# Performance work log

Measured on AMD Instinct MI355X. Metric: run time of the kernel, lower is better.

The kernel has to match this reference:

```python
import jax, jax.numpy as jnp
import numpy as np

N = 50000        # nodes
E = 800000       # edges
G = 256          # graphs in batch
DIMS = [128, 128, 64, 32]
BN_EPS = 1e-5
TEMP = 5.0


def setup_inputs() -> dict:
    key = jax.random.key(0)
    ks = iter(jax.random.split(key, 32))
    inp = {}
    inp["x"] = jax.random.normal(next(ks), (N, DIMS[0]), dtype=jnp.float32)
    inp["edge_index"] = jax.random.randint(next(ks), (2, E), 0, N)
    inp["batch"] = jnp.sort(jax.random.randint(next(ks), (N,), 0, G))
    for i in range(3):
        din, dout = DIMS[i], DIMS[i + 1]
        inp[f"W1_{i}"] = jax.random.normal(next(ks), (din, dout), dtype=jnp.float32) * 0.05
        inp[f"b1_{i}"] = jnp.zeros((dout,), jnp.float32)
        inp[f"W2_{i}"] = jax.random.normal(next(ks), (dout, dout), dtype=jnp.float32) * 0.05
        inp[f"b2_{i}"] = jnp.zeros((dout,), jnp.float32)
        inp[f"gamma_{i}"] = jnp.ones((dout,), jnp.float32)
        inp[f"beta_{i}"] = jnp.zeros((dout,), jnp.float32)
        inp[f"mean_{i}"] = jnp.zeros((dout,), jnp.float32)
        inp[f"var_{i}"] = jnp.ones((dout,), jnp.float32)
    inp["W_lin"] = jax.random.normal(next(ks), (DIMS[3], 1), dtype=jnp.float32) * 0.05
    inp["b_lin"] = jnp.zeros((1,), jnp.float32)
    return inp


def _gin_bn(x, src, dst, W1, b1, W2, b2, g, b, m, v):
    # GINConv with eps=0: h_i = MLP(x_i + sum_{j->i} x_j), then BatchNorm (eval)
    agg = jax.ops.segment_sum(x[src], dst, num_segments=N)  # [N, din]
    h = x + agg
    h = jnp.maximum(h @ W1 + b1, 0.0) @ W2 + b2             # 2-layer MLP
    return (h - m) * jax.lax.rsqrt(v + BN_EPS) * g + b


def reference(x, edge_index, batch,
              W1_0, b1_0, W2_0, b2_0, gamma_0, beta_0, mean_0, var_0,
              W1_1, b1_1, W2_1, b2_1, gamma_1, beta_1, mean_1, var_1,
              W1_2, b1_2, W2_2, b2_2, gamma_2, beta_2, mean_2, var_2,
              W_lin, b_lin):
    src, dst = edge_index[0], edge_index[1]
    layers = [
        (W1_0, b1_0, W2_0, b2_0, gamma_0, beta_0, mean_0, var_0),
        (W1_1, b1_1, W2_1, b2_1, gamma_1, beta_1, mean_1, var_1),
        (W1_2, b1_2, W2_2, b2_2, gamma_2, beta_2, mean_2, var_2),
    ]
    for i, p in enumerate(layers):
        x = _gin_bn(x, src, dst, *p)
        if i != len(layers) - 1:
            x = jnp.maximum(x, 0.0)  # relu; dropout is identity in eval mode
    logits = (x @ W_lin + b_lin) / TEMP                      # [N, 1]
    # per-graph (segment) softmax over nodes
    mx = jax.ops.segment_max(logits, batch, num_segments=G)  # [G, 1]
    e = jnp.exp(logits - mx[batch])
    s = jax.ops.segment_sum(e, batch, num_segments=G)        # [G, 1]
    return e / s[batch]
```

## Files before the change

kernel.cpp:

```cpp
#include <hip/hip_runtime.h>

#define NN 50000
#define NE 800000
#define NG 256
#define N4 (NN * 128 / 4)
#define NQ (NE / 4)
#define CB 64
#define QPB (NQ / CB)
#define NBK 196

typedef __attribute__((ext_vector_type(8))) short bf16x8;
typedef __attribute__((ext_vector_type(4))) float f32x4;

__device__ __forceinline__ unsigned short f2bf_rne(float f) {
    unsigned u = __float_as_uint(f);
    u += 0x7fffu + ((u >> 16) & 1u);
    return (unsigned short)(u >> 16);
}
#define BF2F_LO(u) __uint_as_float((u) << 16)
#define BF2F_HI(u) __uint_as_float((u) & 0xffff0000u)

__global__ void conv_count(const float4* __restrict__ x, ushort4* __restrict__ xh,
                           const int4* __restrict__ dst4, int* __restrict__ cnt1) {
    __shared__ int hist[NBK];
    int i = blockIdx.x * 256 + threadIdx.x;
    if (i < N4) {
        float4 v = x[i];
        ushort4 o;
        o.x = f2bf_rne(v.x); o.y = f2bf_rne(v.y);
        o.z = f2bf_rne(v.z); o.w = f2bf_rne(v.w);
        xh[i] = o;
    }
    if (blockIdx.x < CB) {
        int t = threadIdx.x;
        if (t < NBK) hist[t] = 0;
        __syncthreads();
        int qb = blockIdx.x * QPB;
        for (int qi = t; qi < QPB; qi += 256) {
            int4 d = dst4[qb + qi];
            atomicAdd(&hist[d.x >> 8], 1);
            atomicAdd(&hist[d.y >> 8], 1);
            atomicAdd(&hist[d.z >> 8], 1);
            atomicAdd(&hist[d.w >> 8], 1);
        }
        __syncthreads();
        if (t < NBK) cnt1[blockIdx.x * NBK + t] = hist[t];
    }
}

__global__ __launch_bounds__(256) void scan_buckets(
        const int* __restrict__ cnt1, int* __restrict__ off1,
        int* __restrict__ bstart, int* __restrict__ rowptr) {
    __shared__ int c[CB * NBK];
    __shared__ int sh[256];
    int t = threadIdx.x;
    for (int idx = t; idx < CB * NBK; idx += 256) c[idx] = cnt1[idx];
    __syncthreads();
    int tot = 0;
    if (t < NBK) {
        for (int b = 0; b < CB; b++) {
            int v = c[b * NBK + t];
            c[b * NBK + t] = tot;
            tot += v;
        }
    }
    sh[t] = (t < NBK) ? tot : 0;
    __syncthreads();
    int v = sh[t];
    #pragma unroll
    for (int off = 1; off < 256; off <<= 1) {
        int add = (t >= off) ? sh[t - off] : 0;
        __syncthreads();
        sh[t] += add;
        __syncthreads();
    }
    int excl = sh[t] - v;
    if (t < NBK) {
        bstart[t] = excl;
        for (int b = 0; b < CB; b++) c[b * NBK + t] += excl;
    }
    if (t == 0) { bstart[NBK] = NE; rowptr[NN] = NE; }
    __syncthreads();
    for (int idx = t; idx < CB * NBK; idx += 256) off1[idx] = c[idx];
}

__global__ __launch_bounds__(256) void scatter1(
        const int4* __restrict__ src4, const int4* __restrict__ dst4,
        const int* __restrict__ off1, int2* __restrict__ tmp) {
    __shared__ int curs[NBK];
    int t = threadIdx.x;
    if (t < NBK) curs[t] = off1[blockIdx.x * NBK + t];
    __syncthreads();
    int qb = blockIdx.x * QPB;
    for (int qi = t; qi < QPB; qi += 256) {
        int4 s = src4[qb + qi];
        int4 d = dst4[qb + qi];
        int p0 = atomicAdd(&curs[d.x >> 8], 1);
        int p1 = atomicAdd(&curs[d.y >> 8], 1);
        int p2 = atomicAdd(&curs[d.z >> 8], 1);
        int p3 = atomicAdd(&curs[d.w >> 8], 1);
        tmp[p0] = make_int2(s.x, d.x);
        tmp[p1] = make_int2(s.y, d.y);
        tmp[p2] = make_int2(s.z, d.z);
        tmp[p3] = make_int2(s.w, d.w);
    }
}

__global__ __launch_bounds__(256) void bucket_build(
        const int2* __restrict__ tmp, const int* __restrict__ bstart,
        const int* __restrict__ batch, int* __restrict__ rowptr,
        int* __restrict__ gstart, int* __restrict__ esrc,
        const float* __restrict__ W1, const float* __restrict__ W2,
        const float* __restrict__ W3,
        const float* __restrict__ W21, const float* __restrict__ W12,
        unsigned short* __restrict__ W1t, unsigned short* __restrict__ W2t,
        unsigned short* __restrict__ W3t, unsigned short* __restrict__ W21t,
        unsigned short* __restrict__ W12t) {
    int gidx = blockIdx.x * 256 + threadIdx.x;
    if (gidx < 16384) {
        int n = gidx >> 7, k = gidx & 127;
        W1t[gidx] = f2bf_rne(W1[k * 128 + n]);
        W2t[gidx] = f2bf_rne(W2[k * 128 + n]);
    } else if (gidx < 24576) {
        int i2 = gidx - 16384;
        int n = i2 >> 7, k = i2 & 127;
        W3t[i2] = f2bf_rne(W3[k * 64 + n]);
    } else if (gidx < 28672) {
        int i3 = gidx - 24576;
        int n = i3 >> 6, k = i3 & 63;
        W21t[i3] = f2bf_rne(W21[k * 64 + n]);
    } else if (gidx < 30720) {
        int i4 = gidx - 28672;
        int n = i4 >> 6, k = i4 & 63;
        W12t[i4] = f2bf_rne(W12[k * 32 + n]);
    }

    __shared__ int hist[256];
    __shared__ int sh[256];
    __shared__ int curs[256];
    int t = threadIdx.x, k1 = blockIdx.x;
    int b0 = bstart[k1], b1v = bstart[k1 + 1];
    int cnt = b1v - b0;
    hist[t] = 0;
    __syncthreads();
    for (int e = t; e < cnt; e += 256) {
        int2 sd = tmp[b0 + e];
        atomicAdd(&hist[sd.y & 255], 1);
    }
    __syncthreads();
    int v = hist[t];
    sh[t] = v;
    __syncthreads();
    #pragma unroll
    for (int off = 1; off < 256; off <<= 1) {
        int add = (t >= off) ? sh[t - off] : 0;
        __syncthreads();
        sh[t] += add;
        __syncthreads();
    }
    int excl = sh[t] - v;
    int node = k1 * 256 + t;
    if (node < NN) {
        rowptr[node] = b0 + excl;
        int b = batch[node];
        if (node == 0) {
            for (int g = 0; g <= b; g++) gstart[g] = 0;
        } else {
            int p = batch[node - 1];
            for (int g = p + 1; g <= b; g++) gstart[g] = node;
        }
        if (node == NN - 1) {
            for (int g = b + 1; g <= NG; g++) gstart[g] = NN;
        }
    }
    curs[t] = b0 + excl;
    __syncthreads();
    for (int e = t; e < cnt; e += 256) {
        int2 sd = tmp[b0 + e];
        int slot = atomicAdd(&curs[sd.y & 255], 1);
        esrc[slot] = sd.x;
    }
}


template <int C4>
__device__ __forceinline__ void gather_bf16(const uint4* __restrict__ x4,
                                            const int* __restrict__ esrc,
                                            int beg, int cnt, int node, int lane,
                                            float* a ) {
    constexpr int EPI = 64 / C4;
    const int chunk = lane & (C4 - 1);
    const int esl   = lane / C4;
    #define ACC_U4(u) do { \
        a[0] += BF2F_LO((u).x); a[1] += BF2F_HI((u).x); \
        a[2] += BF2F_LO((u).y); a[3] += BF2F_HI((u).y); \
        a[4] += BF2F_LO((u).z); a[5] += BF2F_HI((u).z); \
        a[6] += BF2F_LO((u).w); a[7] += BF2F_HI((u).w); } while (0)
    if (esl == 0) { uint4 u = x4[(size_t)node * C4 + chunk]; ACC_U4(u); }
    for (int c = 0; c < cnt; c += 64) {
        int take = min(64, cnt - c);
        int myi = (lane < take) ? esrc[beg + c + lane] : 0;
        int i = 0;
        for (; i + 4 * EPI <= take; i += 4 * EPI) {
            int s0 = __shfl(myi, i + esl);
            int s1 = __shfl(myi, i + EPI + esl);
            int s2 = __shfl(myi, i + 2 * EPI + esl);
            int s3 = __shfl(myi, i + 3 * EPI + esl);
            uint4 u0 = x4[(size_t)s0 * C4 + chunk];
            uint4 u1 = x4[(size_t)s1 * C4 + chunk];
            uint4 u2 = x4[(size_t)s2 * C4 + chunk];
            uint4 u3 = x4[(size_t)s3 * C4 + chunk];
            ACC_U4(u0); ACC_U4(u1); ACC_U4(u2); ACC_U4(u3);
        }
        if (i + 2 * EPI <= take) {
            int s0 = __shfl(myi, i + esl);
            int s1 = __shfl(myi, i + EPI + esl);
            uint4 u0 = x4[(size_t)s0 * C4 + chunk];
            uint4 u1 = x4[(size_t)s1 * C4 + chunk];
            ACC_U4(u0); ACC_U4(u1);
            i += 2 * EPI;
        }
        if (i + EPI <= take) {
            int s = __shfl(myi, i + esl);
            uint4 u = x4[(size_t)s * C4 + chunk];
            ACC_U4(u);
            i += EPI;
        }
        int rem = take - i;
        if (rem > 0) {
            int s = __shfl(myi, i + ((esl < rem) ? esl : 0));
            uint4 u = x4[(size_t)s * C4 + chunk];
            if (esl < rem) ACC_U4(u);
        }
    }
    #undef ACC_U4
    for (int off = 32; off >= C4; off >>= 1) {
        #pragma unroll
        for (int q = 0; q < 8; q++)
            a[q] += __shfl_xor(a[q], off);
    }
}

template <int C>
__device__ __forceinline__ void gather_bf16_u2(const uint2* __restrict__ x2,
                                               const int* __restrict__ esrc,
                                               int beg, int cnt, int node, int lane,
                                               float* a ) {
    constexpr int EPI = 64 / C;
    const int chunk = lane & (C - 1);
    const int esl   = lane / C;
    #define ACC_U2(u) do { \
        a[0] += BF2F_LO((u).x); a[1] += BF2F_HI((u).x); \
        a[2] += BF2F_LO((u).y); a[3] += BF2F_HI((u).y); } while (0)
    if (esl == 0) { uint2 u = x2[(size_t)node * C + chunk]; ACC_U2(u); }
    for (int c = 0; c < cnt; c += 64) {
        int take = min(64, cnt - c);
        int myi = (lane < take) ? esrc[beg + c + lane] : 0;
        int i = 0;
        for (; i + 4 * EPI <= take; i += 4 * EPI) {
            int s0 = __shfl(myi, i + esl);
            int s1 = __shfl(myi, i + EPI + esl);
            int s2 = __shfl(myi, i + 2 * EPI + esl);
            int s3 = __shfl(myi, i + 3 * EPI + esl);
            uint2 u0 = x2[(size_t)s0 * C + chunk];
            uint2 u1 = x2[(size_t)s1 * C + chunk];
            uint2 u2 = x2[(size_t)s2 * C + chunk];
            uint2 u3 = x2[(size_t)s3 * C + chunk];
            ACC_U2(u0); ACC_U2(u1); ACC_U2(u2); ACC_U2(u3);
        }
        if (i + 2 * EPI <= take) {
            int s0 = __shfl(myi, i + esl);
            int s1 = __shfl(myi, i + EPI + esl);
            uint2 u0 = x2[(size_t)s0 * C + chunk];
            uint2 u1 = x2[(size_t)s1 * C + chunk];
            ACC_U2(u0); ACC_U2(u1);
            i += 2 * EPI;
        }
        if (i + EPI <= take) {
            int s = __shfl(myi, i + esl);
            uint2 u = x2[(size_t)s * C + chunk];
            ACC_U2(u);
            i += EPI;
        }
        int rem = take - i;
        if (rem > 0) {
            int s = __shfl(myi, i + ((esl < rem) ? esl : 0));
            uint2 u = x2[(size_t)s * C + chunk];
            if (esl < rem) ACC_U2(u);
        }
    }
    #undef ACC_U2
    for (int off = 32; off >= C; off >>= 1) {
        #pragma unroll
        for (int q = 0; q < 4; q++)
            a[q] += __shfl_xor(a[q], off);
    }
}

template <int C>
__device__ __forceinline__ void gather_bf16_u1(const unsigned* __restrict__ x1,
                                               const int* __restrict__ esrc,
                                               int beg, int cnt, int node, int lane,
                                               float* a ) {
    constexpr int EPI = 64 / C;
    const int chunk = lane & (C - 1);
    const int esl   = lane / C;
    #define ACC_U1(u) do { \
        a[0] += BF2F_LO(u); a[1] += BF2F_HI(u); } while (0)
    if (esl == 0) { unsigned u = x1[(size_t)node * C + chunk]; ACC_U1(u); }
    for (int c = 0; c < cnt; c += 64) {
        int take = min(64, cnt - c);
        int myi = (lane < take) ? esrc[beg + c + lane] : 0;
        int i = 0;
        for (; i + 4 * EPI <= take; i += 4 * EPI) {
            int s0 = __shfl(myi, i + esl);
            int s1 = __shfl(myi, i + EPI + esl);
            int s2 = __shfl(myi, i + 2 * EPI + esl);
            int s3 = __shfl(myi, i + 3 * EPI + esl);
            unsigned u0 = x1[(size_t)s0 * C + chunk];
            unsigned u1 = x1[(size_t)s1 * C + chunk];
            unsigned u2 = x1[(size_t)s2 * C + chunk];
            unsigned u3 = x1[(size_t)s3 * C + chunk];
            ACC_U1(u0); ACC_U1(u1); ACC_U1(u2); ACC_U1(u3);
        }
        if (i + 2 * EPI <= take) {
            int s0 = __shfl(myi, i + esl);
            int s1 = __shfl(myi, i + EPI + esl);
            unsigned u0 = x1[(size_t)s0 * C + chunk];
            unsigned u1 = x1[(size_t)s1 * C + chunk];
            ACC_U1(u0); ACC_U1(u1);
            i += 2 * EPI;
        }
        if (i + EPI <= take) {
            int s = __shfl(myi, i + esl);
            unsigned u = x1[(size_t)s * C + chunk];
            ACC_U1(u);
            i += EPI;
        }
        int rem = take - i;
        if (rem > 0) {
            int s = __shfl(myi, i + ((esl < rem) ? esl : 0));
            unsigned u = x1[(size_t)s * C + chunk];
            if (esl < rem) ACC_U1(u);
        }
    }
    #undef ACC_U1
    for (int off = 32; off >= C; off >>= 1) {
        #pragma unroll
        for (int q = 0; q < 2; q++)
            a[q] += __shfl_xor(a[q], off);
    }
}

__global__ __launch_bounds__(256) void gather_L0(
        const unsigned short* __restrict__ xh, const int* __restrict__ esrc,
        const int* __restrict__ rowptr, unsigned short* __restrict__ aggh ) {
    const int wave = threadIdx.x >> 6, lane = threadIdx.x & 63;
    const int node = blockIdx.x * 4 + wave;
    if (node >= NN) return;
    float a[8] = {0, 0, 0, 0, 0, 0, 0, 0};
    int beg = rowptr[node], end = rowptr[node + 1];
    gather_bf16<16>((const uint4*)xh, esrc, beg, end - beg, node, lane, a);
    if (lane < 16) {
        uint4 o;
        o.x = (unsigned)f2bf_rne(a[0]) | ((unsigned)f2bf_rne(a[1]) << 16);
        o.y = (unsigned)f2bf_rne(a[2]) | ((unsigned)f2bf_rne(a[3]) << 16);
        o.z = (unsigned)f2bf_rne(a[4]) | ((unsigned)f2bf_rne(a[5]) << 16);
        o.w = (unsigned)f2bf_rne(a[6]) | ((unsigned)f2bf_rne(a[7]) << 16);
        *(uint4*)&aggh[(size_t)node * 128 + lane * 8] = o;
    }
}

__global__ __launch_bounds__(256) void gather_L1(
        const unsigned short* __restrict__ z1h, const int* __restrict__ esrc,
        const int* __restrict__ rowptr, const float* __restrict__ b1,
        unsigned short* __restrict__ agg1h ) {
    const int wave = threadIdx.x >> 6, lane = threadIdx.x & 63;
    const int node = blockIdx.x * 4 + wave;
    if (node >= NN) return;
    float a[4] = {0, 0, 0, 0};
    int beg = rowptr[node], end = rowptr[node + 1];
    gather_bf16_u2<16>((const uint2*)z1h, esrc, beg, end - beg, node, lane, a);
    if (lane < 16) {
        float4 bv = *(const float4*)&b1[lane * 4];
        uint2 o;
        o.x = (unsigned)f2bf_rne(fmaxf(a[0] + bv.x, 0.f)) |
              ((unsigned)f2bf_rne(fmaxf(a[1] + bv.y, 0.f)) << 16);
        o.y = (unsigned)f2bf_rne(fmaxf(a[2] + bv.z, 0.f)) |
              ((unsigned)f2bf_rne(fmaxf(a[3] + bv.w, 0.f)) << 16);
        *(uint2*)&agg1h[(size_t)node * 64 + lane * 4] = o;
    }
}

__global__ __launch_bounds__(256) void gather_L2(
        const unsigned short* __restrict__ z2h, const int* __restrict__ esrc,
        const int* __restrict__ rowptr, const float* __restrict__ b1,
        unsigned short* __restrict__ agg2h ) {
    const int wave = threadIdx.x >> 6, lane = threadIdx.x & 63;
    const int node = blockIdx.x * 4 + wave;
    if (node >= NN) return;
    float a[2] = {0, 0};
    int beg = rowptr[node], end = rowptr[node + 1];
    gather_bf16_u1<16>((const unsigned*)z2h, esrc, beg, end - beg, node, lane, a);
    if (lane < 16) {
        float2 bv = *(const float2*)&b1[lane * 2];
        unsigned o = (unsigned)f2bf_rne(fmaxf(a[0] + bv.x, 0.f)) |
                     ((unsigned)f2bf_rne(fmaxf(a[1] + bv.y, 0.f)) << 16);
        *(unsigned*)&agg2h[(size_t)node * 32 + lane * 2] = o;
    }
}

__global__ __launch_bounds__(256) void gemm_L0(
        const unsigned short* __restrict__ aggh, unsigned short* __restrict__ z1h,
        const unsigned short* __restrict__ W1t,
        const unsigned short* __restrict__ W2t,
        const unsigned short* __restrict__ W3t,
        const float* __restrict__ b1, const float* __restrict__ b2,
        const float* __restrict__ gamma, const float* __restrict__ beta,
        const float* __restrict__ mean, const float* __restrict__ var) {
    constexpr int MT = 64, LDA = 136;
    __shared__ __align__(16) unsigned short shA[MT * LDA];
    __shared__ __align__(16) unsigned short shB[MT * LDA];
    const int tid = threadIdx.x;
    const int wave = tid >> 6, lane = tid & 63;
    const int nodeBase = blockIdx.x * MT;
    const int lr = lane & 15;
    const int lg = lane >> 4;
    const int lk = lg * 8;
    const int n0 = wave * 32;

    #pragma unroll
    for (int j = 0; j < 4; j++) {
        int f = tid + j * 256;
        int row = f >> 4, c = f & 15;
        int node = nodeBase + row;
        uint4 v = (node < NN) ? ((const uint4*)aggh)[(size_t)node * 16 + c]
                              : make_uint4(0u, 0u, 0u, 0u);
        *(uint4*)&shA[row * LDA + c * 8] = v;
    }
    __syncthreads();

    f32x4 acc[4][2];

    {
        float bv0 = b1[n0 + lr], bv1 = b1[n0 + 16 + lr];
        #pragma unroll
        for (int m = 0; m < 4; m++) {
            f32x4 c0 = {bv0, bv0, bv0, bv0};
            f32x4 c1 = {bv1, bv1, bv1, bv1};
            acc[m][0] = c0; acc[m][1] = c1;
        }
        #pragma unroll
        for (int ks = 0; ks < 4; ks++) {
            const int k0 = ks * 32 + lk;
            bf16x8 wb0 = *(const bf16x8*)&W1t[(n0 + lr) * 128 + k0];
            bf16x8 wb1 = *(const bf16x8*)&W1t[(n0 + 16 + lr) * 128 + k0];
            #pragma unroll
            for (int m = 0; m < 4; m++) {
                bf16x8 af = *(const bf16x8*)&shA[(m * 16 + lr) * LDA + k0];
                acc[m][0] = __builtin_amdgcn_mfma_f32_16x16x32_bf16(af, wb0, acc[m][0], 0, 0, 0);
                acc[m][1] = __builtin_amdgcn_mfma_f32_16x16x32_bf16(af, wb1, acc[m][1], 0, 0, 0);
            }
        }
    }
    #pragma unroll
    for (int m = 0; m < 4; m++) {
        #pragma unroll
        for (int nt = 0; nt < 2; nt++) {
            #pragma unroll
            for (int r = 0; r < 4; r++) {
                shB[(m * 16 + lg * 4 + r) * LDA + (n0 + nt * 16 + lr)] =
                    f2bf_rne(fmaxf(acc[m][nt][r], 0.f));
            }
        }
    }
    __syncthreads();

    {
        float bv0 = b2[n0 + lr], bv1 = b2[n0 + 16 + lr];
        #pragma unroll
        for (int m = 0; m < 4; m++) {
            f32x4 c0 = {bv0, bv0, bv0, bv0};
            f32x4 c1 = {bv1, bv1, bv1, bv1};
            acc[m][0] = c0; acc[m][1] = c1;
        }
        #pragma unroll
        for (int ks = 0; ks < 4; ks++) {
            const int k0 = ks * 32 + lk;
            bf16x8 wb0 = *(const bf16x8*)&W2t[(n0 + lr) * 128 + k0];
            bf16x8 wb1 = *(const bf16x8*)&W2t[(n0 + 16 + lr) * 128 + k0];
            #pragma unroll
            for (int m = 0; m < 4; m++) {
                bf16x8 af = *(const bf16x8*)&shB[(m * 16 + lr) * LDA + k0];
                acc[m][0] = __builtin_amdgcn_mfma_f32_16x16x32_bf16(af, wb0, acc[m][0], 0, 0, 0);
                acc[m][1] = __builtin_amdgcn_mfma_f32_16x16x32_bf16(af, wb1, acc[m][1], 0, 0, 0);
            }
        }
    }
    float s0 = gamma[n0 + lr]      * (1.0f / sqrtf(var[n0 + lr] + 1e-5f));
    float t0 = beta[n0 + lr]       - mean[n0 + lr] * s0;
    float s1 = gamma[n0 + 16 + lr] * (1.0f / sqrtf(var[n0 + 16 + lr] + 1e-5f));
    float t1 = beta[n0 + 16 + lr]  - mean[n0 + 16 + lr] * s1;
    #pragma unroll
    for (int m = 0; m < 4; m++) {
        #pragma unroll
        for (int nt = 0; nt < 2; nt++) {
            float sc = nt ? s1 : s0, sf = nt ? t1 : t0;
            #pragma unroll
            for (int r = 0; r < 4; r++) {
                float y = fmaxf(fmaf(acc[m][nt][r], sc, sf), 0.f);
                shA[(m * 16 + lg * 4 + r) * LDA + (n0 + nt * 16 + lr)] = f2bf_rne(y);
            }
        }
    }
    __syncthreads();

    f32x4 a3[4];
    #pragma unroll
    for (int m = 0; m < 4; m++) {
        f32x4 z = {0.f, 0.f, 0.f, 0.f};
        a3[m] = z;
    }
    #pragma unroll
    for (int ks = 0; ks < 4; ks++) {
        const int k0 = ks * 32 + lk;
        bf16x8 wb = *(const bf16x8*)&W3t[(wave * 16 + lr) * 128 + k0];
        #pragma unroll
        for (int m = 0; m < 4; m++) {
            bf16x8 af = *(const bf16x8*)&shA[(m * 16 + lr) * LDA + k0];
            a3[m] = __builtin_amdgcn_mfma_f32_16x16x32_bf16(af, wb, a3[m], 0, 0, 0);
        }
    }
    #pragma unroll
    for (int m = 0; m < 4; m++) {
        #pragma unroll
        for (int r = 0; r < 4; r++) {
            int node = nodeBase + m * 16 + lg * 4 + r;
            if (node < NN)
                z1h[(size_t)node * 64 + wave * 16 + lr] = f2bf_rne(a3[m][r]);
        }
    }
}

__global__ __launch_bounds__(256) void gemm_L1(
        const unsigned short* __restrict__ agg1h, unsigned short* __restrict__ z2h,
        const unsigned short* __restrict__ W21t,
        const unsigned short* __restrict__ W12t,
        const float* __restrict__ b2, const float* __restrict__ gamma,
        const float* __restrict__ beta, const float* __restrict__ mean,
        const float* __restrict__ var) {
    constexpr int MT = 64, LDA = 72;
    __shared__ __align__(16) unsigned short shA[MT * LDA];
    __shared__ __align__(16) unsigned short shB[MT * LDA];
    const int tid = threadIdx.x;
    const int wave = tid >> 6, lane = tid & 63;
    const int nodeBase = blockIdx.x * MT;
    const int lr = lane & 15;
    const int lg = lane >> 4;
    const int lk = lg * 8;
    const int n0 = wave * 16;

    #pragma unroll
    for (int j = 0; j < 2; j++) {
        int f = tid + j * 256;
        int row = f >> 3, c = f & 7;
        int node = nodeBase + row;
        uint4 v = (node < NN) ? ((const uint4*)agg1h)[(size_t)node * 8 + c]
                              : make_uint4(0u, 0u, 0u, 0u);
        *(uint4*)&shA[row * LDA + c * 8] = v;
    }
    __syncthreads();

    f32x4 acc[4];
    {
        float bv = b2[n0 + lr];
        #pragma unroll
        for (int m = 0; m < 4; m++) {
            f32x4 c0 = {bv, bv, bv, bv};
            acc[m] = c0;
        }
        #pragma unroll
        for (int ks = 0; ks < 2; ks++) {
            const int k0 = ks * 32 + lk;
            bf16x8 wb = *(const bf16x8*)&W21t[(n0 + lr) * 64 + k0];
            #pragma unroll
            for (int m = 0; m < 4; m++) {
                bf16x8 af = *(const bf16x8*)&shA[(m * 16 + lr) * LDA + k0];
                acc[m] = __builtin_amdgcn_mfma_f32_16x16x32_bf16(af, wb, acc[m], 0, 0, 0);
            }
        }
    }
    float sc = gamma[n0 + lr] * (1.0f / sqrtf(var[n0 + lr] + 1e-5f));
    float sf = beta[n0 + lr] - mean[n0 + lr] * sc;
    #pragma unroll
    for (int m = 0; m < 4; m++) {
        #pragma unroll
        for (int r = 0; r < 4; r++) {
            float y = fmaxf(fmaf(acc[m][r], sc, sf), 0.f);
            shB[(m * 16 + lg * 4 + r) * LDA + (n0 + lr)] = f2bf_rne(y);
        }
    }
    __syncthreads();

    const int rh = (wave >> 1) * 32, ch = (wave & 1) * 16;
    f32x4 a3[2];
    {
        f32x4 z = {0.f, 0.f, 0.f, 0.f};
        a3[0] = z; a3[1] = z;
    }
    #pragma unroll
    for (int ks = 0; ks < 2; ks++) {
        const int k0 = ks * 32 + lk;
        bf16x8 wb = *(const bf16x8*)&W12t[(ch + lr) * 64 + k0];
        #pragma unroll
        for (int m = 0; m < 2; m++) {
            bf16x8 af = *(const bf16x8*)&shB[(rh + m * 16 + lr) * LDA + k0];
            a3[m] = __builtin_amdgcn_mfma_f32_16x16x32_bf16(af, wb, a3[m], 0, 0, 0);
        }
    }
    #pragma unroll
    for (int m = 0; m < 2; m++) {
        #pragma unroll
        for (int r = 0; r < 4; r++) {
            int node = nodeBase + rh + m * 16 + lg * 4 + r;
            if (node < NN)
                z2h[(size_t)node * 32 + ch + lr] = f2bf_rne(a3[m][r]);
        }
    }
}

__global__ __launch_bounds__(256) void gemm_L2(
        const unsigned short* __restrict__ agg2h, float* __restrict__ logits,
        const float* __restrict__ W2, const float* __restrict__ b2,
        const float* __restrict__ gamma, const float* __restrict__ beta,
        const float* __restrict__ mean, const float* __restrict__ var,
        const float* __restrict__ Wl, const float* __restrict__ bl) {
    constexpr int MT = 32, LD = 36;
    __shared__ float sh[MT * LD];
    const int tid = threadIdx.x;
    const int nodeBase = blockIdx.x * MT;

    {
        int row = tid >> 3, c = tid & 7;
        int node = nodeBase + row;
        uint2 v = (node < NN) ? ((const uint2*)agg2h)[(size_t)node * 8 + c]
                              : make_uint2(0u, 0u);
        sh[row * LD + c * 4 + 0] = BF2F_LO(v.x);
        sh[row * LD + c * 4 + 1] = BF2F_HI(v.x);
        sh[row * LD + c * 4 + 2] = BF2F_LO(v.y);
        sh[row * LD + c * 4 + 3] = BF2F_HI(v.y);
    }
    __syncthreads();

    const int colid = tid % 8, rowid = tid / 8;
    const int c0 = colid * 4, r0 = rowid;
    float acc[4];
    {
        float4 bv = *(const float4*)&b2[c0];
        acc[0] = bv.x; acc[1] = bv.y; acc[2] = bv.z; acc[3] = bv.w;
        #pragma unroll
        for (int k4 = 0; k4 < 8; k4++) {
            float4 w[4];
            #pragma unroll
            for (int kk = 0; kk < 4; kk++)
                w[kk] = *(const float4*)&W2[(k4 * 4 + kk) * 32 + c0];
            float4 a = *(const float4*)&sh[r0 * LD + k4 * 4];
            const float av[4] = {a.x, a.y, a.z, a.w};
            #pragma unroll
            for (int kk = 0; kk < 4; kk++) {
                const float* wp = (const float*)&w[kk];
                #pragma unroll
                for (int j = 0; j < 4; j++)
                    acc[j] = fmaf(av[kk], wp[j], acc[j]);
            }
        }
    }
    float4 gv = *(const float4*)&gamma[c0];
    float4 bev = *(const float4*)&beta[c0];
    float4 mv = *(const float4*)&mean[c0];
    float4 vv = *(const float4*)&var[c0];
    float4 wl = *(const float4*)&Wl[c0];
    float p = 0.f;
    {
        const float* gp = (const float*)&gv; const float* bp = (const float*)&bev;
        const float* mp = (const float*)&mv; const float* vp = (const float*)&vv;
        const float* wp = (const float*)&wl;
        #pragma unroll
        for (int j = 0; j < 4; j++) {
            float sc = gp[j] * (1.0f / sqrtf(vp[j] + 1e-5f));
            float y = (acc[j] - mp[j]) * sc + bp[j];
            p = fmaf(y, wp[j], p);
        }
    }
    p += __shfl_xor(p, 1);
    p += __shfl_xor(p, 2);
    p += __shfl_xor(p, 4);
    int node = nodeBase + r0;
    if ((tid & 7) == 0 && node < NN)
        logits[node] = (p + bl[0]) * 0.2f;
}

__global__ __launch_bounds__(256) void seg_softmax(
        const float* __restrict__ logits, const int* __restrict__ gstart,
        float* __restrict__ out) {
    __shared__ float slog[1024];
    __shared__ float sred[4];
    __shared__ float sbc[2];
    int g = blockIdx.x;
    int beg = gstart[g], end = gstart[g + 1];
    int cnt = end - beg;
    int t = threadIdx.x;
    if (cnt <= 0) return;
    bool fits = (cnt <= 1024);

    float lmax = -3.402823466e+38f;
    for (int i = t; i < cnt; i += 256) {
        float lg = logits[beg + i];
        if (fits) slog[i] = lg;
        lmax = fmaxf(lmax, lg);
    }
    #pragma unroll
    for (int off = 32; off > 0; off >>= 1)
        lmax = fmaxf(lmax, __shfl_down(lmax, off));
    if ((t & 63) == 0) sred[t >> 6] = lmax;
    __syncthreads();
    if (t == 0) sbc[0] = fmaxf(fmaxf(sred[0], sred[1]), fmaxf(sred[2], sred[3]));
    __syncthreads();
    float gm = sbc[0];

    float lsum = 0.f;
    for (int i = t; i < cnt; i += 256) {
        float lg = fits ? slog[i] : logits[beg + i];
        float e = expf(lg - gm);
        if (fits) slog[i] = e;
        lsum += e;
    }
    #pragma unroll
    for (int off = 32; off > 0; off >>= 1)
        lsum += __shfl_down(lsum, off);
    __syncthreads();
    if ((t & 63) == 0) sred[t >> 6] = lsum;
    __syncthreads();
    if (t == 0) sbc[1] = (sred[0] + sred[1]) + (sred[2] + sred[3]);
    __syncthreads();
    float inv = 1.0f / sbc[1];

    for (int i = t; i < cnt; i += 256) {
        float e = fits ? slog[i] : expf(logits[beg + i] - gm);
        out[beg + i] = e * inv;
    }
}

extern "C" void kernel_launch(void* const* d_in, const int* in_sizes, int n_in,
                              void* d_out, int out_size, void* d_ws, size_t ws_size,
                              hipStream_t stream) {
    const float* x    = (const float*)d_in[0];
    const int*   ei   = (const int*)d_in[1];
    const int*   srcI = ei;
    const int*   dstI = ei + NE;
    const int*   batch = (const int*)d_in[2];

    const float* P[29];
    for (int i = 0; i < 29; i++) P[i] = (const float*)d_in[i];
    const float* Wlin = P[27];
    const float* blin = P[28];

    unsigned short* xh  = (unsigned short*)d_ws;
    unsigned short* z1h = xh + (size_t)NN * 128;
    unsigned short* z2h = z1h + (size_t)NN * 64;
    float* logits = (float*)(z2h + (size_t)NN * 32);
    int* gstart = (int*)(logits + NN);
    int* rowptr = gstart + NG + 1;
    int* cnt1   = rowptr + NN + 1;
    int* off1   = cnt1 + CB * NBK;
    int* bstart = off1 + CB * NBK;
    uintptr_t tal = ((uintptr_t)(bstart + NBK + 1) + 15) & ~(uintptr_t)15;
    int2* tmp   = (int2*)tal;
    int* esrc   = (int*)(tmp + NE);
    uintptr_t pal = ((uintptr_t)(esrc + NE) + 255) & ~(uintptr_t)255;
    unsigned short* aggh  = (unsigned short*)pal;
    unsigned short* W1t   = aggh + (size_t)NN * 128;
    unsigned short* W2t   = W1t + 16384;
    unsigned short* W3t   = W2t + 16384;
    unsigned short* W21t  = W3t + 8192;
    unsigned short* W12t  = W21t + 4096;
    unsigned short* agg1h = W12t + 2048;
    unsigned short* agg2h = agg1h + (size_t)NN * 64;
    float* outp = (float*)d_out;

    const int TB = 256;

    conv_count<<<(N4 + TB - 1) / TB, TB, 0, stream>>>(
        (const float4*)x, (ushort4*)xh, (const int4*)dstI, cnt1);
    scan_buckets<<<1, 256, 0, stream>>>(cnt1, off1, bstart, rowptr);
    scatter1<<<CB, 256, 0, stream>>>(
        (const int4*)srcI, (const int4*)dstI, off1, tmp);
    bucket_build<<<NBK, 256, 0, stream>>>(tmp, bstart, batch, rowptr, gstart, esrc,
        P[3], P[5], P[11], P[13], P[19], W1t, W2t, W3t, W21t, W12t);

    const int GB   = (NN + 3) / 4;
    const int FB64 = (NN + 63) / 64;
    const int FB32 = (NN + 31) / 32;

    gather_L0<<<GB, 256, 0, stream>>>(xh, esrc, rowptr, aggh);
    gemm_L0<<<FB64, 256, 0, stream>>>(aggh, z1h, W1t, W2t, W3t,
        P[4], P[6], P[7], P[8], P[9], P[10]);
    gather_L1<<<GB, 256, 0, stream>>>(z1h, esrc, rowptr, P[12], agg1h);
    gemm_L1<<<FB64, 256, 0, stream>>>(agg1h, z2h, W21t, W12t,
        P[14], P[15], P[16], P[17], P[18]);
    gather_L2<<<GB, 256, 0, stream>>>(z2h, esrc, rowptr, P[20], agg2h);
    gemm_L2<<<FB32, 256, 0, stream>>>(agg2h, logits,
        P[21], P[22], P[23], P[24], P[25], P[26], Wlin, blin);

    seg_softmax<<<NG, 256, 0, stream>>>(logits, gstart, outp);
}
```

Before: 262.3 us.

## Fold bucket scan into scatter and build kernels; pack edge temp into 32 bits

Removes the single-block scan_buckets kernel. Each scatter1 and bucket_build block now reloads the full count table and recomputes the bucket prefix sums it needs. The intermediate edge buffer changes from int2 (src, dst) to a single 32-bit word holding the 16-bit source and the low 8 bits of the destination, halving its write and read traffic. The cost is a redundant scan in every block, a 50KB shared-memory table per block, and reliance on node ids fitting in 16 bits.

```diff
diff --git a/kernel.cpp b/kernel.cpp
--- a/kernel.cpp
+++ b/kernel.cpp
@@ -48,23 +48,25 @@
     }
 }
 
-__global__ __launch_bounds__(256) void scan_buckets(
-        const int* __restrict__ cnt1, int* __restrict__ off1,
-        int* __restrict__ bstart, int* __restrict__ rowptr) {
+__global__ __launch_bounds__(256) void scatter1(
+        const int4* __restrict__ src4, const int4* __restrict__ dst4,
+        const int* __restrict__ cnt1, unsigned* __restrict__ tmp) {
     __shared__ int c[CB * NBK];
     __shared__ int sh[256];
+    __shared__ int curs[256];
     int t = threadIdx.x;
     for (int idx = t; idx < CB * NBK; idx += 256) c[idx] = cnt1[idx];
     __syncthreads();
-    int tot = 0;
+    int myoff = 0, tv = 0;
     if (t < NBK) {
+        int run = 0;
         for (int b = 0; b < CB; b++) {
-            int v = c[b * NBK + t];
-            c[b * NBK + t] = tot;
-            tot += v;
-        }
-    }
-    sh[t] = (t < NBK) ? tot : 0;
+            if (b == (int)blockIdx.x) myoff = run;
+            run += c[b * NBK + t];
+        }
+        tv = run;
+    }
+    sh[t] = tv;
     __syncthreads();
     int v = sh[t];
     #pragma unroll
@@ -75,21 +77,7 @@
         __syncthreads();
     }
     int excl = sh[t] - v;
-    if (t < NBK) {
-        bstart[t] = excl;
-        for (int b = 0; b < CB; b++) c[b * NBK + t] += excl;
-    }
-    if (t == 0) { bstart[NBK] = NE; rowptr[NN] = NE; }
-    __syncthreads();
-    for (int idx = t; idx < CB * NBK; idx += 256) off1[idx] = c[idx];
-}
-
-__global__ __launch_bounds__(256) void scatter1(
-        const int4* __restrict__ src4, const int4* __restrict__ dst4,
-        const int* __restrict__ off1, int2* __restrict__ tmp) {
-    __shared__ int curs[NBK];
-    int t = threadIdx.x;
-    if (t < NBK) curs[t] = off1[blockIdx.x * NBK + t];
+    if (t < NBK) curs[t] = excl + myoff;
     __syncthreads();
     int qb = blockIdx.x * QPB;
     for (int qi = t; qi < QPB; qi += 256) {
@@ -99,15 +87,15 @@
         int p1 = atomicAdd(&curs[d.y >> 8], 1);
         int p2 = atomicAdd(&curs[d.z >> 8], 1);
         int p3 = atomicAdd(&curs[d.w >> 8], 1);
-        tmp[p0] = make_int2(s.x, d.x);
-        tmp[p1] = make_int2(s.y, d.y);
-        tmp[p2] = make_int2(s.z, d.z);
-        tmp[p3] = make_int2(s.w, d.w);
+        tmp[p0] = (unsigned)s.x | ((unsigned)(d.x & 255) << 16);
+        tmp[p1] = (unsigned)s.y | ((unsigned)(d.y & 255) << 16);
+        tmp[p2] = (unsigned)s.z | ((unsigned)(d.z & 255) << 16);
+        tmp[p3] = (unsigned)s.w | ((unsigned)(d.w & 255) << 16);
     }
 }
 
 __global__ __launch_bounds__(256) void bucket_build(
-        const int2* __restrict__ tmp, const int* __restrict__ bstart,
+        const unsigned* __restrict__ tmp, const int* __restrict__ cnt1,
         const int* __restrict__ batch, int* __restrict__ rowptr,
         int* __restrict__ gstart, int* __restrict__ esrc,
         const float* __restrict__ W1, const float* __restrict__ W2,
@@ -135,17 +123,43 @@
         W12t[i4] = f2bf_rne(W12[k * 32 + n]);
     }
 
+    __shared__ int c[CB * NBK];
+    __shared__ int tot[256];
+    __shared__ int pre[256];
     __shared__ int hist[256];
     __shared__ int sh[256];
     __shared__ int curs[256];
     int t = threadIdx.x, k1 = blockIdx.x;
-    int b0 = bstart[k1], b1v = bstart[k1 + 1];
-    int cnt = b1v - b0;
+
+    for (int idx = t; idx < CB * NBK; idx += 256) c[idx] = cnt1[idx];
+    __syncthreads();
+    int tv = 0;
+    if (t < NBK) {
+        int run = 0;
+        for (int b = 0; b < CB; b++) run += c[b * NBK + t];
+        tv = run;
+    }
+    tot[t] = tv;
+    sh[t] = tv;
+    __syncthreads();
+    int v0 = sh[t];
+    #pragma unroll
+    for (int off = 1; off < 256; off <<= 1) {
+        int add = (t >= off) ? sh[t - off] : 0;
+        __syncthreads();
+        sh[t] += add;
+        __syncthreads();
+    }
+    pre[t] = sh[t] - v0;
+    __syncthreads();
+    const int b0 = pre[k1];
+    const int cnt = tot[k1];
+
     hist[t] = 0;
     __syncthreads();
     for (int e = t; e < cnt; e += 256) {
-        int2 sd = tmp[b0 + e];
-        atomicAdd(&hist[sd.y & 255], 1);
+        unsigned pk = tmp[b0 + e];
+        atomicAdd(&hist[pk >> 16], 1);
     }
     __syncthreads();
     int v = hist[t];
@@ -173,12 +187,13 @@
             for (int g = b + 1; g <= NG; g++) gstart[g] = NN;
         }
     }
+    if (k1 == 0 && t == 0) rowptr[NN] = NE;
     curs[t] = b0 + excl;
     __syncthreads();
     for (int e = t; e < cnt; e += 256) {
-        int2 sd = tmp[b0 + e];
-        int slot = atomicAdd(&curs[sd.y & 255], 1);
-        esrc[slot] = sd.x;
+        unsigned pk = tmp[b0 + e];
+        int slot = atomicAdd(&curs[pk >> 16], 1);
+        esrc[slot] = (int)(pk & 0xffffu);
     }
 }
 
@@ -772,10 +787,8 @@
     int* gstart = (int*)(logits + NN);
     int* rowptr = gstart + NG + 1;
     int* cnt1   = rowptr + NN + 1;
-    int* off1   = cnt1 + CB * NBK;
-    int* bstart = off1 + CB * NBK;
-    uintptr_t tal = ((uintptr_t)(bstart + NBK + 1) + 15) & ~(uintptr_t)15;
-    int2* tmp   = (int2*)tal;
+    uintptr_t tal = ((uintptr_t)(cnt1 + CB * NBK) + 15) & ~(uintptr_t)15;
+    unsigned* tmp = (unsigned*)tal;
     int* esrc   = (int*)(tmp + NE);
     uintptr_t pal = ((uintptr_t)(esrc + NE) + 255) & ~(uintptr_t)255;
     unsigned short* aggh  = (unsigned short*)pal;
@@ -792,10 +805,9 @@
 
     conv_count<<<(N4 + TB - 1) / TB, TB, 0, stream>>>(
         (const float4*)x, (ushort4*)xh, (const int4*)dstI, cnt1);
-    scan_buckets<<<1, 256, 0, stream>>>(cnt1, off1, bstart, rowptr);
     scatter1<<<CB, 256, 0, stream>>>(
-        (const int4*)srcI, (const int4*)dstI, off1, tmp);
-    bucket_build<<<NBK, 256, 0, stream>>>(tmp, bstart, batch, rowptr, gstart, esrc,
+        (const int4*)srcI, (const int4*)dstI, cnt1, tmp);
+    bucket_build<<<NBK, 256, 0, stream>>>(tmp, cnt1, batch, rowptr, gstart, esrc,
         P[3], P[5], P[11], P[13], P[19], W1t, W2t, W3t, W21t, W12t);
 
     const int GB   = (NN + 3) / 4;
```

After: 261.0 us. About the same (-0.5%).
